# Kernel optimization log

Hardware: AMD Instinct MI355X
Metric: run time of the kernel (lower is better)

## Reference

```python
import jax, jax.numpy as jnp
from jax import lax
import numpy as np

N_TOTAL = 262144
NUM_SAMPLE = 1024
KNN_K = 16
NUM_CLASSES = 13
HIDDEN = 128
EPS = 1e-8


def _sqdist(a, b):
    # (Na,3),(Nb,3) -> (Na,Nb) squared euclidean; same argmin as torch.cdist
    return (jnp.sum(a * a, axis=1)[:, None]
            + jnp.sum(b * b, axis=1)[None, :]
            - 2.0 * a @ b.T)


def _farthest_point_sample(xyz, n_samples):
    # sequential FPS starting from index 0 (deterministic start)
    n = xyz.shape[0]

    def step(carry, _):
        min_d2, last = carry
        d2 = jnp.sum((xyz - xyz[last]) ** 2, axis=-1)
        min_d2 = jnp.minimum(min_d2, d2)
        nxt = jnp.argmax(min_d2).astype(jnp.int32)
        return (min_d2, nxt), nxt

    init = (jnp.full((n,), 1e10, dtype=xyz.dtype), jnp.int32(0))
    _, idxs = lax.scan(step, init, None, length=n_samples - 1)
    return jnp.concatenate([jnp.zeros((1,), jnp.int32), idxs])


def _compute_normals(pts, k):
    # PCA normal per point from its k nearest neighbors (self excluded)
    d2 = _sqdist(pts, pts)                      # (S,S), S=1024 -> small
    _, nbr_idx = lax.top_k(-d2, k + 1)
    nbr = pts[nbr_idx[:, 1:]]                   # (S,k,3)
    centered = nbr - jnp.mean(nbr, axis=1, keepdims=True)
    cov = jnp.einsum('ski,skj->sij', centered, centered) / (k - 1)
    _, eigvecs = jnp.linalg.eigh(cov)           # ascending eigenvalues
    normal = eigvecs[..., 0]                    # smallest-eigval eigenvector
    return normal / (jnp.linalg.norm(normal, axis=-1, keepdims=True) + EPS)


def _forward(gaussian_positions, gaussian_colors, W1, b1, W2, b2, W3, b3):
    sample_idx = _farthest_point_sample(gaussian_positions, NUM_SAMPLE)
    dxyz = gaussian_positions[sample_idx]       # (S,3)
    drgb = gaussian_colors[sample_idx]          # (S,3)
    dnrm = _compute_normals(dxyz, KNN_K)        # (S,3)
    feats = jnp.concatenate([dxyz, drgb, dnrm], axis=1)  # (S,9)

    # pointwise segmentation network (stand-in for PointNet++ get_model)
    h = jax.nn.relu(feats @ W1 + b1)
    h = jax.nn.relu(h @ W2 + b2)
    pred = h @ W3 + b3                          # (S, num_classes)

    feat_down = jax.nn.softmax(pred, axis=1)
    lbl_down = jnp.argmax(pred, axis=1)

    # 1-NN label propagation: streaming-min candidate (memory-bound)
    d2_full = _sqdist(gaussian_positions, dxyz)  # (N, S) ~ 1 GB
    nearest = jnp.argmin(d2_full, axis=1)
    return feat_down[nearest], lbl_down[nearest]


def setup_inputs() -> dict:
    key = jax.random.key(0)
    ks = jax.random.split(key, 8)
    pos = jax.random.normal(ks[0], (N_TOTAL, 3), jnp.float32)
    col = jax.random.uniform(ks[1], (N_TOTAL, 3), jnp.float32)
    W1 = jax.random.normal(ks[2], (9, HIDDEN), jnp.float32) / np.sqrt(9.0)
    b1 = jnp.zeros((HIDDEN,), jnp.float32)
    W2 = jax.random.normal(ks[3], (HIDDEN, HIDDEN), jnp.float32) / np.sqrt(HIDDEN)
    b2 = jnp.zeros((HIDDEN,), jnp.float32)
    W3 = jax.random.normal(ks[4], (HIDDEN, NUM_CLASSES), jnp.float32) / np.sqrt(HIDDEN)
    b3 = jnp.zeros((NUM_CLASSES,), jnp.float32)
    return {"gaussian_positions": pos, "gaussian_colors": col,
            "W1": W1, "b1": b1, "W2": W2, "b2": b2, "W3": W3, "b3": b3}


def reference(gaussian_positions, gaussian_colors, W1, b1, W2, b2, W3, b3):
    return _forward(gaussian_positions, gaussian_colors, W1, b1, W2, b2, W3, b3)
```

## Files before the change

### kernel.cpp

```cpp
#include <hip/hip_runtime.h>
#include <math.h>

#define N_TOTAL    262144
#define NUM_SAMPLE 1024
#define FPS_BLOCKS 64
#define FPS_THREADS 256
#define FPS_PPT (N_TOTAL / (FPS_BLOCKS * FPS_THREADS))
#define M_WAVE 4
#define POOL (FPS_BLOCKS * 4 * M_WAVE)
#define ENT_PER_T (POOL / FPS_THREADS)
#define QD (POOL / 64)
#define SEL_CAP 1023

__device__ __forceinline__ float addrn(float a, float b) { return __fadd_rn(a, b); }
__device__ __forceinline__ float subrn(float a, float b) { return __fsub_rn(a, b); }
__device__ __forceinline__ float mulrn(float a, float b) { return __fmul_rn(a, b); }

__device__ __forceinline__ float d2rn(float ax, float ay, float az,
                                      float bx, float by, float bz) {
  float dx = subrn(ax, bx), dy = subrn(ay, by), dz = subrn(az, bz);
  return addrn(addrn(mulrn(dx, dx), mulrn(dy, dy)), mulrn(dz, dz));
}

__device__ __forceinline__ bool lex_gt(float m1, unsigned i1, float m2, unsigned i2) {
  return (m1 > m2) || (m1 == m2 && i1 > i2);
}
__device__ __forceinline__ bool lex_ge(float m1, unsigned i1, float m2, unsigned i2) {
  return (m1 > m2) || (m1 == m2 && i1 >= i2);
}

template <int CTRL>
__device__ __forceinline__ int dpp_i(int x) {
  return __builtin_amdgcn_update_dpp(x, x, CTRL, 0xF, 0xF, false);
}
__device__ __forceinline__ float wave_fmax_bcast(float v) {
  v = fmaxf(v, __int_as_float(dpp_i<0x111>(__float_as_int(v))));
  v = fmaxf(v, __int_as_float(dpp_i<0x112>(__float_as_int(v))));
  v = fmaxf(v, __int_as_float(dpp_i<0x114>(__float_as_int(v))));
  v = fmaxf(v, __int_as_float(dpp_i<0x118>(__float_as_int(v))));
  v = fmaxf(v, __int_as_float(dpp_i<0x142>(__float_as_int(v))));
  v = fmaxf(v, __int_as_float(dpp_i<0x143>(__float_as_int(v))));
  return __int_as_float(__builtin_amdgcn_readlane(__float_as_int(v), 63));
}
__device__ __forceinline__ unsigned wave_umax_bcast(unsigned v) {
  unsigned o;
  o = (unsigned)dpp_i<0x111>((int)v); v = (o > v) ? o : v;
  o = (unsigned)dpp_i<0x112>((int)v); v = (o > v) ? o : v;
  o = (unsigned)dpp_i<0x114>((int)v); v = (o > v) ? o : v;
  o = (unsigned)dpp_i<0x118>((int)v); v = (o > v) ? o : v;
  o = (unsigned)dpp_i<0x142>((int)v); v = (o > v) ? o : v;
  o = (unsigned)dpp_i<0x143>((int)v); v = (o > v) ? o : v;
  return (unsigned)__builtin_amdgcn_readlane((int)v, 63);
}

__device__ __forceinline__ float slapy2f(float x, float y) {
  float xa = fabsf(x), ya = fabsf(y);
  float w = fmaxf(xa, ya), z = fminf(xa, ya);
  if (z == 0.f) return w;
  float t = z / w;
  return w * __fsqrt_rn(1.f + t * t);
}

__device__ __forceinline__ void slartgf(float f, float g, float& c, float& s, float& r) {
  if (g == 0.f) { c = 1.f; s = 0.f; r = f; }
  else if (f == 0.f) { c = 0.f; s = (g > 0.f) ? 1.f : -1.f; r = fabsf(g); }
  else {
    float d = __fsqrt_rn(f * f + g * g);
    c = fabsf(f) / d;
    r = (f >= 0.f) ? d : -d;
    s = g / r;
  }
}

__device__ void slaev2f(float a, float b, float c0, float& rt1, float& rt2,
                        float& cs1, float& sn1) {
  float sm = a + c0, df = a - c0;
  float adf = fabsf(df), tb = b + b, ab = fabsf(tb);
  float acmx, acmn;
  if (fabsf(a) > fabsf(c0)) { acmx = a; acmn = c0; } else { acmx = c0; acmn = a; }
  float rt;
  if (adf > ab)      { float t = ab / adf; rt = adf * __fsqrt_rn(1.f + t * t); }
  else if (adf < ab) { float t = adf / ab; rt = ab * __fsqrt_rn(1.f + t * t); }
  else               { rt = ab * __fsqrt_rn(2.f); }
  int sgn1;
  if (sm < 0.f)      { rt1 = 0.5f * (sm - rt); sgn1 = -1; rt2 = (acmx / rt1) * acmn - (b / rt1) * b; }
  else if (sm > 0.f) { rt1 = 0.5f * (sm + rt); sgn1 = 1;  rt2 = (acmx / rt1) * acmn - (b / rt1) * b; }
  else               { rt1 = 0.5f * rt; rt2 = -0.5f * rt; sgn1 = 1; }
  float cs; int sgn2;
  if (df >= 0.f) { cs = df + rt; sgn2 = 1; } else { cs = df - rt; sgn2 = -1; }
  float acs = fabsf(cs);
  if (acs > ab) {
    float ct = -tb / cs;
    sn1 = 1.f / __fsqrt_rn(1.f + ct * ct);
    cs1 = ct * sn1;
  } else {
    if (ab == 0.f) { cs1 = 1.f; sn1 = 0.f; }
    else { float tn = -cs / tb; cs1 = 1.f / __fsqrt_rn(1.f + tn * tn); sn1 = tn * cs1; }
  }
  if (sgn1 == sgn2) { float tn = cs1; cs1 = -sn1; sn1 = tn; }
}

#define D_(i) d[(i)-1]
#define E_(i) e[(i)-1]

__device__ void ssteqr3(float d[3], float e[2], float Z[3][3]) {
  const float eps    = 5.9604645e-08f;
  const float eps2   = 3.5527137e-15f;
  const float safmin = 1.17549435e-38f;
  const float ssfmax = 3.0744573e+18f;
  const float ssfmin = 3.0517578e-05f;
  const int n = 3;
  int jtot = 0, nmaxit = 90;
  int l1 = 1;

  while (true) {
    if (l1 > n) break;
    if (l1 > 1) E_(l1 - 1) = 0.f;
    int m = n;
    for (int mm = l1; mm <= n - 1; ++mm) {
      float tst = fabsf(E_(mm));
      if (tst == 0.f) { m = mm; break; }
      if (tst <= (__fsqrt_rn(fabsf(D_(mm))) * __fsqrt_rn(fabsf(D_(mm + 1)))) * eps) {
        E_(mm) = 0.f; m = mm; break;
      }
    }
    int l = l1, lsv = l, lend = m, lendsv = m;
    l1 = m + 1;
    if (lend == l) continue;

    float anorm = fabsf(D_(lend));
    for (int i2 = l; i2 <= lend - 1; ++i2) {
      anorm = fmaxf(anorm, fabsf(D_(i2)));
      anorm = fmaxf(anorm, fabsf(E_(i2)));
    }
    int iscale = 0;
    if (anorm == 0.f) continue;
    if (anorm > ssfmax) {
      iscale = 1; float mul = ssfmax / anorm;
      for (int i2 = l; i2 <= lend; ++i2) D_(i2) *= mul;
      for (int i2 = l; i2 <= lend - 1; ++i2) E_(i2) *= mul;
    } else if (anorm < ssfmin) {
      iscale = 2; float mul = ssfmin / anorm;
      for (int i2 = l; i2 <= lend; ++i2) D_(i2) *= mul;
      for (int i2 = l; i2 <= lend - 1; ++i2) E_(i2) *= mul;
    }

    if (fabsf(D_(lend)) < fabsf(D_(l))) { int t = l; l = lend; lend = t; }

    if (lend > l) {
      while (true) {
        int m2 = lend;
        if (l != lend) {
          for (int mm = l; mm <= lend - 1; ++mm) {
            float tst = fabsf(E_(mm)); tst = tst * tst;
            if (tst <= (eps2 * fabsf(D_(mm))) * fabsf(D_(mm + 1)) + safmin) { m2 = mm; break; }
          }
        }
        if (m2 < lend) E_(m2) = 0.f;
        float p = D_(l);
        if (m2 == l) { D_(l) = p; l = l + 1; if (l <= lend) continue; break; }
        if (m2 == l + 1) {
          float rt1, rt2, cc, ss;
          slaev2f(D_(l), E_(l), D_(l + 1), rt1, rt2, cc, ss);
          for (int i2 = 0; i2 < 3; ++i2) {
            float tmp = Z[i2][l];
            Z[i2][l]     = cc * tmp - ss * Z[i2][l - 1];
            Z[i2][l - 1] = ss * tmp + cc * Z[i2][l - 1];
          }
          D_(l) = rt1; D_(l + 1) = rt2; E_(l) = 0.f;
          l = l + 2; if (l <= lend) continue; break;
        }
        if (jtot == nmaxit) break;
        ++jtot;
        float g = (D_(l + 1) - p) / (2.f * E_(l));
        float r = slapy2f(g, 1.f);
        float sgn_rg = (g >= 0.f) ? r : -r;
        g = D_(m2) - p + E_(l) / (g + sgn_rg);
        float s = 1.f, c = 1.f;
        p = 0.f;
        float csv[2], ssv[2];
        for (int i2 = m2 - 1; i2 >= l; --i2) {
          float f = s * E_(i2);
          float b = c * E_(i2);
          slartgf(g, f, c, s, r);
          if (i2 != m2 - 1) E_(i2 + 1) = r;
          g = D_(i2 + 1) - p;
          r = (D_(i2) - g) * s + 2.f * c * b;
          p = s * r;
          D_(i2 + 1) = g + p;
          g = c * r - b;
          csv[i2 - l] = c; ssv[i2 - l] = -s;
        }
        for (int j = m2 - 1; j >= l; --j) {
          float ct = csv[j - l], st = ssv[j - l];
          for (int i2 = 0; i2 < 3; ++i2) {
            float tmp = Z[i2][j];
            Z[i2][j]     = ct * tmp - st * Z[i2][j - 1];
            Z[i2][j - 1] = st * tmp + ct * Z[i2][j - 1];
          }
        }
        D_(l) = D_(l) - p;
        E_(l) = g;
      }
    } else {
      while (true) {
        int m2 = lend;
        if (l != lend) {
          for (int mm = l; mm >= lend + 1; --mm) {
            float tst = fabsf(E_(mm - 1)); tst = tst * tst;
            if (tst <= (eps2 * fabsf(D_(mm))) * fabsf(D_(mm - 1)) + safmin) { m2 = mm; break; }
          }
        }
        if (m2 > lend) E_(m2 - 1) = 0.f;
        float p = D_(l);
        if (m2 == l) { D_(l) = p; l = l - 1; if (l >= lend) continue; break; }
        if (m2 == l - 1) {
          float rt1, rt2, cc, ss;
          slaev2f(D_(l - 1), E_(l - 1), D_(l), rt1, rt2, cc, ss);
          for (int i2 = 0; i2 < 3; ++i2) {
            float tmp = Z[i2][l - 1];
            Z[i2][l - 1] = cc * tmp - ss * Z[i2][l - 2];
            Z[i2][l - 2] = ss * tmp + cc * Z[i2][l - 2];
          }
          D_(l - 1) = rt1; D_(l) = rt2; E_(l - 1) = 0.f;
          l = l - 2; if (l >= lend) continue; break;
        }
        if (jtot == nmaxit) break;
        ++jtot;
        float g = (D_(l - 1) - p) / (2.f * E_(l - 1));
        float r = slapy2f(g, 1.f);
        float sgn_rg = (g >= 0.f) ? r : -r;
        g = D_(m2) - p + E_(l - 1) / (g + sgn_rg);
        float s = 1.f, c = 1.f;
        p = 0.f;
        float csv[2], ssv[2];
        for (int i2 = m2; i2 <= l - 1; ++i2) {
          float f = s * E_(i2);
          float b = c * E_(i2);
          slartgf(g, f, c, s, r);
          if (i2 != m2) E_(i2 - 1) = r;
          g = D_(i2) - p;
          r = (D_(i2 + 1) - g) * s + 2.f * c * b;
          p = s * r;
          D_(i2) = g + p;
          g = c * r - b;
          csv[i2 - m2] = c; ssv[i2 - m2] = s;
        }
        for (int j = m2; j <= l - 1; ++j) {
          float ct = csv[j - m2], st = ssv[j - m2];
          for (int i2 = 0; i2 < 3; ++i2) {
            float tmp = Z[i2][j];
            Z[i2][j]     = ct * tmp - st * Z[i2][j - 1];
            Z[i2][j - 1] = st * tmp + ct * Z[i2][j - 1];
          }
        }
        D_(l) = D_(l) - p;
        E_(l - 1) = g;
      }
    }
    if (iscale == 1) {
      float mul = anorm / ssfmax;
      for (int i2 = lsv; i2 <= lendsv; ++i2) D_(i2) *= mul;
      for (int i2 = lsv; i2 <= lendsv - 1; ++i2) E_(i2) *= mul;
    } else if (iscale == 2) {
      float mul = anorm / ssfmin;
      for (int i2 = lsv; i2 <= lendsv; ++i2) D_(i2) *= mul;
      for (int i2 = lsv; i2 <= lendsv - 1; ++i2) E_(i2) *= mul;
    }
  }
  for (int ii = 2; ii <= n; ++ii) {
    int i2 = ii - 1, k = i2;
    float p = D_(i2);
    for (int j = ii; j <= n; ++j) if (D_(j) < p) { k = j; p = D_(j); }
    if (k != i2) {
      D_(k) = D_(i2); D_(i2) = p;
      for (int rr = 0; rr < 3; ++rr) {
        float t = Z[rr][i2 - 1]; Z[rr][i2 - 1] = Z[rr][k - 1]; Z[rr][k - 1] = t;
      }
    }
  }
}

__device__ void eigh3_smallest(float a00, float a10, float a20, float a11, float a21, float a22,
                               float& nx, float& ny, float& nz) {
  float d[3], e[2];
  float Z[3][3] = {{1.f,0.f,0.f},{0.f,1.f,0.f},{0.f,0.f,1.f}};
  float tau, v2;
  {
    float alpha = a10, x = a20;
    float xnorm = fabsf(x);
    if (xnorm == 0.f) {
      tau = 0.f; v2 = 0.f;
      d[0] = a00; d[1] = a11; d[2] = a22;
      e[0] = alpha; e[1] = a21;
    } else {
      float beta = -copysignf(slapy2f(alpha, x), alpha);
      tau = (beta - alpha) / beta;
      v2 = x / (alpha - beta);
      float w0 = (tau * a11) + tau * (a21 * v2);
      float w1 = (tau * a21) + (tau * v2) * a22;
      float ac = (-0.5f * tau) * (w0 + w1 * v2);
      w0 = w0 + ac;
      w1 = w1 + ac * v2;
      d[0] = a00;
      d[1] = (a11 - w0) - w0;
      d[2] = (a22 - v2 * w1) - w1 * v2;
      e[0] = beta;
      e[1] = (a21 - v2 * w0) - w1;
    }
  }
  ssteqr3(d, e, Z);
  if (tau != 0.f) {
    for (int c = 0; c < 3; ++c) {
      float w = Z[1][c] + Z[2][c] * v2;
      float temp = (-tau) * w;
      Z[1][c] = Z[1][c] + temp;
      Z[2][c] = Z[2][c] + v2 * temp;
    }
  }
  nx = Z[0][0]; ny = Z[1][0]; nz = Z[2][0];
}

__global__ void k0_init(unsigned long long* cand, int* sample_idx) {
  int t = blockIdx.x * blockDim.x + threadIdx.x;
  if (t < 2 * POOL) cand[t] = 0ull;
  if (t == 0) sample_idx[0] = 0;
}

__global__ __launch_bounds__(FPS_THREADS, 1) void k1_fps(
    const float* __restrict__ pos,
    unsigned long long* __restrict__ cand,
    int* __restrict__ sample_idx) {
  __shared__ float4 sel4[SEL_CAP];
  __shared__ float act_x[POOL], act_y[POOL], act_z[POOL], act_md[POOL];
  __shared__ unsigned act_idf[POOL];
  __shared__ float thrT_md[FPS_THREADS];
  __shared__ unsigned thrT_idf[FPS_THREADS];
  __shared__ int sh_pc;

  const int tidx = threadIdx.x;
  const int lane = tidx & 63;
  const int gtid = blockIdx.x * FPS_THREADS + tidx;

  float px[FPS_PPT], py[FPS_PPT], pz[FPS_PPT], md[FPS_PPT];
#pragma unroll
  for (int k = 0; k < FPS_PPT; ++k) {
    int p = gtid + k * (FPS_BLOCKS * FPS_THREADS);
    px[k] = pos[3 * p]; py[k] = pos[3 * p + 1]; pz[k] = pos[3 * p + 2];
    md[k] = 1e10f;
  }
  const unsigned idf0 = 0x3FFFFFu - (unsigned)gtid;
  if (tidx == 0) sel4[0] = make_float4(pos[0], pos[1], pos[2], 0.f);
  __syncthreads();
  int sel_cnt = 1, total = 0, bt = 0;
  while (total < NUM_SAMPLE - 1) {
    ++bt;
    {
      float4 sc = sel4[0];
      for (int s = 0; s < sel_cnt; ++s) {
        float4 sn = (s + 1 < sel_cnt) ? sel4[s + 1] : sc;
#pragma unroll
        for (int k = 0; k < FPS_PPT; ++k)
          md[k] = fminf(md[k], d2rn(px[k], py[k], pz[k], sc.x, sc.y, sc.z));
        sc = sn;
      }
    }
    const unsigned tag = (unsigned)bt & 1023u;
    unsigned long long* setbase = cand + (size_t)(bt & 1) * POOL;
    {
      float wmd[FPS_PPT];
#pragma unroll
      for (int k = 0; k < FPS_PPT; ++k) wmd[k] = md[k];
      unsigned long long mypub = 0ull;
      for (int r = 0; r < M_WAVE; ++r) {
        float bm = wmd[0]; unsigned bidf = idf0;
#pragma unroll
        for (int k = 1; k < FPS_PPT; ++k) {
          unsigned idfk = idf0 - ((unsigned)k << 14);
          if (wmd[k] > bm || (wmd[k] == bm && idfk > bidf)) { bm = wmd[k]; bidf = idfk; }
        }
        float wmx = wave_fmax_bcast(bm);
        unsigned tb = (bm == wmx) ? bidf : 0u;
        unsigned widf = wave_umax_bcast(tb);
        if (lane == r)
          mypub = ((unsigned long long)__float_as_uint(wmx) << 32) |
                  ((unsigned long long)widf << 10);
#pragma unroll
        for (int k = 0; k < FPS_PPT; ++k) {
          unsigned idfk = idf0 - ((unsigned)k << 14);
          if (wmd[k] == wmx && idfk == widf) wmd[k] = -1.f;
        }
      }
      if (lane < M_WAVE)
        __hip_atomic_store(setbase + blockIdx.x * (4 * M_WAVE) + (tidx >> 6) * M_WAVE + lane,
                           mypub | tag, __ATOMIC_RELAXED, __HIP_MEMORY_SCOPE_AGENT);
    }
    const int base_w = tidx * ENT_PER_T;
    {
      float cmd[ENT_PER_T]; unsigned cidf[ENT_PER_T];
      float cx[ENT_PER_T], cy[ENT_PER_T], cz[ENT_PER_T];
      unsigned done = 0;
      while (done != 0xFu) {
#pragma unroll
        for (int j = 0; j < ENT_PER_T; ++j) {
          if (!((done >> j) & 1u)) {
            unsigned long long v = __hip_atomic_load(setbase + base_w + j,
                                                     __ATOMIC_RELAXED, __HIP_MEMORY_SCOPE_AGENT);
            if ((unsigned)(v & 1023ull) == tag) {
              done |= 1u << j;
              cmd[j] = __uint_as_float((unsigned)(v >> 32));
              cidf[j] = (unsigned)((v >> 10) & 0x3FFFFFull);
              int gidx = 0x3FFFFF - (int)cidf[j];
              cx[j] = pos[3 * gidx]; cy[j] = pos[3 * gidx + 1]; cz[j] = pos[3 * gidx + 2];
            }
          }
        }
        if (done != 0xFu) __builtin_amdgcn_s_sleep(1);
      }
#pragma unroll
      for (int j = 0; j < ENT_PER_T; ++j) {
        int e = j * FPS_THREADS + tidx;
        act_x[e] = cx[j]; act_y[e] = cy[j]; act_z[e] = cz[j];
        act_md[e] = cmd[j]; act_idf[e] = cidf[j];
      }
      thrT_md[tidx] = cmd[ENT_PER_T - 1]; thrT_idf[tidx] = cidf[ENT_PER_T - 1];
    }
    __syncthreads();
    const int room = (NUM_SAMPLE - 1) - total;
    if (tidx < 64) {
      float q_md[QD], q_x[QD], q_y[QD], q_z[QD];
      unsigned q_idf[QD];
#pragma unroll
      for (int r = 0; r < QD; ++r) {
        int e2 = lane + 64 * r;
        q_x[r] = act_x[e2]; q_y[r] = act_y[e2]; q_z[r] = act_z[e2];
        q_md[r] = act_md[e2]; q_idf[r] = act_idf[e2];
      }
      float rm = thrT_md[lane]; unsigned ri = thrT_idf[lane];
#pragma unroll
      for (int r = 1; r < 4; ++r) {
        float m = thrT_md[lane + 64 * r]; unsigned ii = thrT_idf[lane + 64 * r];
        if (lex_gt(m, ii, rm, ri)) { rm = m; ri = ii; }
      }
      float Tmd = wave_fmax_bcast(rm);
      unsigned tbT = (rm == Tmd) ? ri : 0u;
      unsigned Tidf = wave_umax_bcast(tbT);

      int picks = 0;
      float X = 1e30f, Y = 1e30f, Z = 1e30f;
      for (;;) {
        float bm = -1.f; unsigned bidf = 0u;
        float bx = 0.f, by = 0.f, bz = 0.f;
#pragma unroll
        for (int j = 0; j < QD; ++j) {
          float nd = fminf(q_md[j], d2rn(q_x[j], q_y[j], q_z[j], X, Y, Z));
          q_md[j] = nd;
          if (lex_gt(nd, q_idf[j], bm, bidf)) {
            bm = nd; bidf = q_idf[j]; bx = q_x[j]; by = q_y[j]; bz = q_z[j];
          }
        }
        float wmx = wave_fmax_bcast(bm);
        unsigned long long ball = __ballot(bm == wmx);
        unsigned widf; int owner;
        if (__builtin_popcountll(ball) == 1) {
          owner = __builtin_ctzll(ball);
          widf = (unsigned)__builtin_amdgcn_readlane((int)bidf, owner);
        } else {
          unsigned tb = (bm == wmx) ? bidf : 0u;
          widf = wave_umax_bcast(tb);
          owner = __builtin_ctzll(__ballot(bm == wmx && bidf == widf));
        }
        if (picks >= room) break;
        if (!lex_ge(wmx, widf, Tmd, Tidf)) break;
        X = __int_as_float(__builtin_amdgcn_readlane(__float_as_int(bx), owner));
        Y = __int_as_float(__builtin_amdgcn_readlane(__float_as_int(by), owner));
        Z = __int_as_float(__builtin_amdgcn_readlane(__float_as_int(bz), owner));
        if (lane == 0) {
          sel4[picks] = make_float4(X, Y, Z, 0.f);
          if (blockIdx.x == 0) sample_idx[1 + total + picks] = 0x3FFFFF - (int)widf;
        }
        ++picks;
      }
      if (lane == 0) sh_pc = picks;
    }
    __syncthreads();
    sel_cnt = sh_pc;
    total += sel_cnt;
  }
}

__global__ __launch_bounds__(256) void k2a_knn(
    const float* __restrict__ pos, const float* __restrict__ col,
    const int* __restrict__ sample_idx,
    float4* __restrict__ sp4g, float* __restrict__ feats9) {
  __shared__ float4 sp[NUM_SAMPLE];
  const int tid = threadIdx.x, lane = tid & 63, wv = tid >> 6;
  for (int i = tid; i < NUM_SAMPLE; i += 256) {
    int idx = sample_idx[i];
    float x = pos[3 * idx], y = pos[3 * idx + 1], z = pos[3 * idx + 2];
    float nrm = addrn(addrn(mulrn(x, x), mulrn(y, y)), mulrn(z, z));
    float4 v = make_float4(x, y, z, nrm);
    sp[i] = v;
    if (blockIdx.x == 0) sp4g[i] = v;
  }
  __syncthreads();
  for (int it = 0; it < 4; ++it) {
    const int r = blockIdx.x * 16 + wv * 4 + it;
    float4 pr = sp[r];
    unsigned long long kk[16];
#pragma unroll
    for (int k = 0; k < 16; ++k) {
      int j = lane + 64 * k;
      float4 q = sp[j];
      float dot = fmaf(pr.z, q.z, fmaf(pr.y, q.y, mulrn(pr.x, q.x)));
      float d2 = subrn(addrn(pr.w, q.w), mulrn(2.f, dot));
      unsigned b = __float_as_uint(d2);
      unsigned sbits = (b & 0x80000000u) ? ~b : (b | 0x80000000u);
      kk[k] = ((unsigned long long)sbits << 32) | (unsigned)j;
    }
    int bi[17];
#pragma unroll
    for (int rsel = 0; rsel < 17; ++rsel) {
      unsigned long long best = 0xFFFFFFFFFFFFFFFFull;
#pragma unroll
      for (int k = 0; k < 16; ++k) best = (kk[k] < best) ? kk[k] : best;
#pragma unroll
      for (int mk = 1; mk < 64; mk <<= 1) {
        unsigned long long o = (unsigned long long)__shfl_xor((long long)best, mk, 64);
        best = (o < best) ? o : best;
      }
      int j = (int)(best & 0xFFFFFFFFull);
      bi[rsel] = j;
#pragma unroll
      for (int k = 0; k < 16; ++k)
        if (((j >> 6) == k) && ((j & 63) == lane)) kk[k] = 0xFFFFFFFFFFFFFFFFull;
    }
    float mx = 0.f, my = 0.f, mz = 0.f;
#pragma unroll
    for (int k = 1; k <= 16; ++k) {
      float4 q = sp[bi[k]];
      mx = addrn(mx, q.x); my = addrn(my, q.y); mz = addrn(mz, q.z);
    }
    mx = mulrn(mx, 0.0625f); my = mulrn(my, 0.0625f); mz = mulrn(mz, 0.0625f);
    float c00 = 0.f, c01 = 0.f, c02 = 0.f, c11 = 0.f, c12 = 0.f, c22 = 0.f;
#pragma unroll
    for (int k = 1; k <= 16; ++k) {
      float4 q = sp[bi[k]];
      float dx = subrn(q.x, mx), dy = subrn(q.y, my), dz = subrn(q.z, mz);
      c00 = addrn(c00, mulrn(dx, dx)); c01 = addrn(c01, mulrn(dx, dy));
      c02 = addrn(c02, mulrn(dx, dz)); c11 = addrn(c11, mulrn(dy, dy));
      c12 = addrn(c12, mulrn(dy, dz)); c22 = addrn(c22, mulrn(dz, dz));
    }
    c00 /= 15.f; c01 /= 15.f; c02 /= 15.f; c11 /= 15.f; c12 /= 15.f; c22 /= 15.f;

    float n0, n1, n2;
    eigh3_smallest(c00, c01, c02, c11, c12, c22, n0, n1, n2);
    float nn = __fsqrt_rn(addrn(addrn(mulrn(n0, n0), mulrn(n1, n1)), mulrn(n2, n2)));
    float den = addrn(nn, 1e-8f);
    n0 /= den; n1 /= den; n2 /= den;

    if (lane == 0) {
      int myidx = sample_idx[r];
      float* f = feats9 + r * 9;
      f[0] = pr.x; f[1] = pr.y; f[2] = pr.z;
      f[3] = col[3 * myidx]; f[4] = col[3 * myidx + 1]; f[5] = col[3 * myidx + 2];
      f[6] = n0; f[7] = n1; f[8] = n2;
    }
  }
}

__global__ __launch_bounds__(64) void k2b_mlp(
    const float* __restrict__ W1, const float* __restrict__ b1,
    const float* __restrict__ W2, const float* __restrict__ b2,
    const float* __restrict__ W3, const float* __restrict__ b3,
    const float* __restrict__ feats9,
    float* __restrict__ featd, int* __restrict__ lbl) {
  __shared__ float hbuf[64][129];
  const int tid = threadIdx.x;
  const int r = blockIdx.x * 64 + tid;
  float f9[9];
#pragma unroll
  for (int k = 0; k < 9; ++k) f9[k] = feats9[r * 9 + k];
  for (int jo = 0; jo < 128; ++jo) {
    float acc = 0.f;
#pragma unroll
    for (int k = 0; k < 9; ++k) acc = fmaf(f9[k], W1[k * 128 + jo], acc);
    acc += b1[jo];
    hbuf[tid][jo] = fmaxf(acc, 0.f);
  }
  float pd[13];
#pragma unroll
  for (int c = 0; c < 13; ++c) pd[c] = 0.f;
  for (int io = 0; io < 128; io += 16) {
    float acc[16];
#pragma unroll
    for (int t = 0; t < 16; ++t) acc[t] = 0.f;
    for (int j = 0; j < 128; ++j) {
      float hj = hbuf[tid][j];
#pragma unroll
      for (int t = 0; t < 16; ++t) acc[t] = fmaf(hj, W2[j * 128 + io + t], acc[t]);
    }
#pragma unroll
    for (int t = 0; t < 16; ++t) {
      float h2 = fmaxf(acc[t] + b2[io + t], 0.f);
#pragma unroll
      for (int c = 0; c < 13; ++c) pd[c] = fmaf(h2, W3[(io + t) * 13 + c], pd[c]);
    }
  }
#pragma unroll
  for (int c = 0; c < 13; ++c) pd[c] += b3[c];
  float mmax = pd[0];
#pragma unroll
  for (int c = 1; c < 13; ++c) mmax = fmaxf(mmax, pd[c]);
  float es = 0.f, ev[13];
#pragma unroll
  for (int c = 0; c < 13; ++c) { ev[c] = expf(pd[c] - mmax); es += ev[c]; }
#pragma unroll
  for (int c = 0; c < 13; ++c) featd[r * 13 + c] = ev[c] / es;
  int am = 0; float bv = pd[0];
#pragma unroll
  for (int c = 1; c < 13; ++c) { if (pd[c] > bv) { bv = pd[c]; am = c; } }
  lbl[r] = am;
}

__global__ __launch_bounds__(256) void k3_assign(
    const float* __restrict__ pos,
    const float4* __restrict__ sp4g,
    const float* __restrict__ featd,
    const int* __restrict__ lbl,
    float* __restrict__ out) {
  __shared__ float4 sp[NUM_SAMPLE];
  for (int i = threadIdx.x; i < NUM_SAMPLE; i += 256) sp[i] = sp4g[i];
  __syncthreads();
  int i = blockIdx.x * 256 + threadIdx.x;
  float x = pos[3 * i], y = pos[3 * i + 1], z = pos[3 * i + 2];
  float an = addrn(addrn(mulrn(x, x), mulrn(y, y)), mulrn(z, z));
  float bestd = 3.402823466e+38f; int bestj = 0;
#pragma unroll 4
  for (int j = 0; j < NUM_SAMPLE; ++j) {
    float4 q = sp[j];
    float dot = fmaf(z, q.z, fmaf(y, q.y, mulrn(x, q.x)));
    float d2 = subrn(addrn(an, q.w), mulrn(2.f, dot));
    if (d2 < bestd) { bestd = d2; bestj = j; }
  }
  const float* fr = featd + bestj * 13;
  float* o = out + (size_t)i * 13;
#pragma unroll
  for (int c = 0; c < 13; ++c) o[c] = fr[c];
  out[(size_t)N_TOTAL * 13 + i] = (float)lbl[bestj];
}

extern "C" void kernel_launch(void* const* d_in, const int* in_sizes, int n_in,
                              void* d_out, int out_size, void* d_ws, size_t ws_size,
                              hipStream_t stream) {
  (void)in_sizes; (void)n_in; (void)out_size; (void)ws_size;
  const float* pos = (const float*)d_in[0];
  const float* col = (const float*)d_in[1];
  const float* W1 = (const float*)d_in[2];
  const float* b1 = (const float*)d_in[3];
  const float* W2 = (const float*)d_in[4];
  const float* b2 = (const float*)d_in[5];
  const float* W3 = (const float*)d_in[6];
  const float* b3 = (const float*)d_in[7];
  float* out = (float*)d_out;

  char* w = (char*)d_ws;
  unsigned long long* cand = (unsigned long long*)(w);
  int* sample_idx = (int*)(w + 65536);
  float4* sp4g = (float4*)(w + 73728);
  float* featd = (float*)(w + 90112);
  int* lbl = (int*)(w + 143360);
  float* feats9 = (float*)(w + 147456);

  k0_init<<<16, 256, 0, stream>>>(cand, sample_idx);
  k1_fps<<<FPS_BLOCKS, FPS_THREADS, 0, stream>>>(pos, cand, sample_idx);
  k2a_knn<<<64, 256, 0, stream>>>(pos, col, sample_idx, sp4g, feats9);
  k2b_mlp<<<16, 64, 0, stream>>>(W1, b1, W2, b2, W3, b3, feats9, featd, lbl);
  k3_assign<<<N_TOTAL / 256, 256, 0, stream>>>(pos, sp4g, featd, lbl, out);
}
```

Measured before the change: 1.710 ms.

## Double per-wave FPS candidates and pack candidate pool into float4 LDS

```diff
diff --git a/kernel.cpp b/kernel.cpp
--- a/kernel.cpp
+++ b/kernel.cpp
@@ -6,10 +6,10 @@
 #define FPS_BLOCKS 64
 #define FPS_THREADS 256
 #define FPS_PPT (N_TOTAL / (FPS_BLOCKS * FPS_THREADS))
-#define M_WAVE 4
+#define M_WAVE 8
 #define POOL (FPS_BLOCKS * 4 * M_WAVE)
 #define ENT_PER_T (POOL / FPS_THREADS)
-#define QD (POOL / 64)
+#define QL (POOL / 64)
 #define SEL_CAP 1023
 
 __device__ __forceinline__ float addrn(float a, float b) { return __fadd_rn(a, b); }
@@ -332,7 +332,7 @@
     unsigned long long* __restrict__ cand,
     int* __restrict__ sample_idx) {
   __shared__ float4 sel4[SEL_CAP];
-  __shared__ float act_x[POOL], act_y[POOL], act_z[POOL], act_md[POOL];
+  __shared__ float4 act4[POOL];
   __shared__ unsigned act_idf[POOL];
   __shared__ float thrT_md[FPS_THREADS];
   __shared__ unsigned thrT_idf[FPS_THREADS];
@@ -395,16 +395,15 @@
         __hip_atomic_store(setbase + blockIdx.x * (4 * M_WAVE) + (tidx >> 6) * M_WAVE + lane,
                            mypub | tag, __ATOMIC_RELAXED, __HIP_MEMORY_SCOPE_AGENT);
     }
-    const int base_w = tidx * ENT_PER_T;
     {
       float cmd[ENT_PER_T]; unsigned cidf[ENT_PER_T];
       float cx[ENT_PER_T], cy[ENT_PER_T], cz[ENT_PER_T];
       unsigned done = 0;
-      while (done != 0xFu) {
+      while (done != 0xFFu) {
 #pragma unroll
         for (int j = 0; j < ENT_PER_T; ++j) {
           if (!((done >> j) & 1u)) {
-            unsigned long long v = __hip_atomic_load(setbase + base_w + j,
+            unsigned long long v = __hip_atomic_load(setbase + j * FPS_THREADS + tidx,
                                                      __ATOMIC_RELAXED, __HIP_MEMORY_SCOPE_AGENT);
             if ((unsigned)(v & 1023ull) == tag) {
               done |= 1u << j;
@@ -415,26 +414,30 @@
             }
           }
         }
-        if (done != 0xFu) __builtin_amdgcn_s_sleep(1);
+        if (done != 0xFFu) __builtin_amdgcn_s_sleep(1);
       }
 #pragma unroll
       for (int j = 0; j < ENT_PER_T; ++j) {
         int e = j * FPS_THREADS + tidx;
-        act_x[e] = cx[j]; act_y[e] = cy[j]; act_z[e] = cz[j];
-        act_md[e] = cmd[j]; act_idf[e] = cidf[j];
-      }
-      thrT_md[tidx] = cmd[ENT_PER_T - 1]; thrT_idf[tidx] = cidf[ENT_PER_T - 1];
+        act4[e] = make_float4(cx[j], cy[j], cz[j], cmd[j]);
+        act_idf[e] = cidf[j];
+      }
+      float tm = -1.f; unsigned ti = 0u;
+      if ((tidx & 7) == 7) {
+#pragma unroll
+        for (int j = 0; j < ENT_PER_T; ++j)
+          if (lex_gt(cmd[j], cidf[j], tm, ti)) { tm = cmd[j]; ti = cidf[j]; }
+      }
+      thrT_md[tidx] = tm; thrT_idf[tidx] = ti;
     }
     __syncthreads();
     const int room = (NUM_SAMPLE - 1) - total;
     if (tidx < 64) {
-      float q_md[QD], q_x[QD], q_y[QD], q_z[QD];
-      unsigned q_idf[QD];
-#pragma unroll
-      for (int r = 0; r < QD; ++r) {
+      float q_md[QL]; unsigned q_idf[QL];
+#pragma unroll
+      for (int r = 0; r < QL; ++r) {
         int e2 = lane + 64 * r;
-        q_x[r] = act_x[e2]; q_y[r] = act_y[e2]; q_z[r] = act_z[e2];
-        q_md[r] = act_md[e2]; q_idf[r] = act_idf[e2];
+        q_md[r] = act4[e2].w; q_idf[r] = act_idf[e2];
       }
       float rm = thrT_md[lane]; unsigned ri = thrT_idf[lane];
 #pragma unroll
@@ -452,11 +455,12 @@
         float bm = -1.f; unsigned bidf = 0u;
         float bx = 0.f, by = 0.f, bz = 0.f;
 #pragma unroll
-        for (int j = 0; j < QD; ++j) {
-          float nd = fminf(q_md[j], d2rn(q_x[j], q_y[j], q_z[j], X, Y, Z));
+        for (int j = 0; j < QL; ++j) {
+          float4 a = act4[lane + 64 * j];
+          float nd = fminf(q_md[j], d2rn(a.x, a.y, a.z, X, Y, Z));
           q_md[j] = nd;
           if (lex_gt(nd, q_idf[j], bm, bidf)) {
-            bm = nd; bidf = q_idf[j]; bx = q_x[j]; by = q_y[j]; bz = q_z[j];
+            bm = nd; bidf = q_idf[j]; bx = a.x; by = a.y; bz = a.z;
           }
         }
         float wmx = wave_fmax_bcast(bm);
```

Measured after the change: 2.390 ms. 39.8% more time.

## Publish more FPS candidates per wave and compact pool by threshold

Applied to the files above, without the earlier changes.

```diff
diff --git a/kernel.cpp b/kernel.cpp
--- a/kernel.cpp
+++ b/kernel.cpp
@@ -6,10 +6,11 @@
 #define FPS_BLOCKS 64
 #define FPS_THREADS 256
 #define FPS_PPT (N_TOTAL / (FPS_BLOCKS * FPS_THREADS))
-#define M_WAVE 4
+#define M_WAVE 8
 #define POOL (FPS_BLOCKS * 4 * M_WAVE)
 #define ENT_PER_T (POOL / FPS_THREADS)
-#define QD (POOL / 64)
+#define CAP 1024
+#define QD 16
 #define SEL_CAP 1023
 
 __device__ __forceinline__ float addrn(float a, float b) { return __fadd_rn(a, b); }
@@ -332,14 +333,15 @@
     unsigned long long* __restrict__ cand,
     int* __restrict__ sample_idx) {
   __shared__ float4 sel4[SEL_CAP];
-  __shared__ float act_x[POOL], act_y[POOL], act_z[POOL], act_md[POOL];
-  __shared__ unsigned act_idf[POOL];
-  __shared__ float thrT_md[FPS_THREADS];
-  __shared__ unsigned thrT_idf[FPS_THREADS];
-  __shared__ int sh_pc;
+  __shared__ float act_x[CAP], act_y[CAP], act_z[CAP], act_md[CAP];
+  __shared__ unsigned act_idf[CAP];
+  __shared__ float wred_m7[4], wred_m4[4];
+  __shared__ unsigned wred_i7[4], wred_i4[4];
+  __shared__ int sh_cnt, sh_pc;
 
   const int tidx = threadIdx.x;
   const int lane = tidx & 63;
+  const int wv = tidx >> 6;
   const int gtid = blockIdx.x * FPS_THREADS + tidx;
 
   float px[FPS_PPT], py[FPS_PPT], pz[FPS_PPT], md[FPS_PPT];
@@ -392,15 +394,15 @@
         }
       }
       if (lane < M_WAVE)
-        __hip_atomic_store(setbase + blockIdx.x * (4 * M_WAVE) + (tidx >> 6) * M_WAVE + lane,
+        __hip_atomic_store(setbase + blockIdx.x * (4 * M_WAVE) + wv * M_WAVE + lane,
                            mypub | tag, __ATOMIC_RELAXED, __HIP_MEMORY_SCOPE_AGENT);
     }
     const int base_w = tidx * ENT_PER_T;
+    float cmd[ENT_PER_T]; unsigned cidf[ENT_PER_T];
+    float cx[ENT_PER_T], cy[ENT_PER_T], cz[ENT_PER_T];
     {
-      float cmd[ENT_PER_T]; unsigned cidf[ENT_PER_T];
-      float cx[ENT_PER_T], cy[ENT_PER_T], cz[ENT_PER_T];
       unsigned done = 0;
-      while (done != 0xFu) {
+      while (done != 0xFFu) {
 #pragma unroll
         for (int j = 0; j < ENT_PER_T; ++j) {
           if (!((done >> j) & 1u)) {
@@ -415,37 +417,75 @@
             }
           }
         }
-        if (done != 0xFu) __builtin_amdgcn_s_sleep(1);
-      }
+        if (done != 0xFFu) __builtin_amdgcn_s_sleep(1);
+      }
+    }
+    {
+      float m7 = cmd[ENT_PER_T - 1]; unsigned i7 = cidf[ENT_PER_T - 1];
+      float w7 = wave_fmax_bcast(m7);
+      unsigned t7 = (m7 == w7) ? i7 : 0u;
+      unsigned wi7 = wave_umax_bcast(t7);
+      float m4 = cmd[4]; unsigned i4 = cidf[4];
+      float w4 = wave_fmax_bcast(m4);
+      unsigned t4 = (m4 == w4) ? i4 : 0u;
+      unsigned wi4 = wave_umax_bcast(t4);
+      if (lane == 0) { wred_m7[wv] = w7; wred_i7[wv] = wi7; wred_m4[wv] = w4; wred_i4[wv] = wi4; }
+      if (tidx == 0) sh_cnt = 0;
+    }
+    __syncthreads();
+    float Tmd = wred_m7[0]; unsigned Tidf = wred_i7[0];
+    float T2m = wred_m4[0]; unsigned T2i = wred_i4[0];
+#pragma unroll
+    for (int w = 1; w < 4; ++w) {
+      if (lex_gt(wred_m7[w], wred_i7[w], Tmd, Tidf)) { Tmd = wred_m7[w]; Tidf = wred_i7[w]; }
+      if (lex_gt(wred_m4[w], wred_i4[w], T2m, T2i)) { T2m = wred_m4[w]; T2i = wred_i4[w]; }
+    }
+    unsigned fl = 0; int myc = 0;
+#pragma unroll
+    for (int j = 0; j < ENT_PER_T; ++j) {
+      if (lex_ge(cmd[j], cidf[j], Tmd, Tidf)) { fl |= 1u << j; ++myc; }
+    }
+    int base = atomicAdd(&sh_cnt, myc);
+    __syncthreads();
+    const int cnt = sh_cnt;
+    const bool ovf = (cnt > CAP);
+    if (!ovf) {
+      int s = base;
 #pragma unroll
       for (int j = 0; j < ENT_PER_T; ++j) {
-        int e = j * FPS_THREADS + tidx;
-        act_x[e] = cx[j]; act_y[e] = cy[j]; act_z[e] = cz[j];
-        act_md[e] = cmd[j]; act_idf[e] = cidf[j];
-      }
-      thrT_md[tidx] = cmd[ENT_PER_T - 1]; thrT_idf[tidx] = cidf[ENT_PER_T - 1];
+        if ((fl >> j) & 1u) {
+          act_x[s] = cx[j]; act_y[s] = cy[j]; act_z[s] = cz[j];
+          act_md[s] = cmd[j]; act_idf[s] = cidf[j];
+          ++s;
+        }
+      }
+    } else {
+#pragma unroll
+      for (int k = 0; k < 4; ++k) {
+        int s = tidx * 4 + k;
+        act_x[s] = cx[k]; act_y[s] = cy[k]; act_z[s] = cz[k];
+        act_md[s] = cmd[k]; act_idf[s] = cidf[k];
+      }
     }
     __syncthreads();
     const int room = (NUM_SAMPLE - 1) - total;
     if (tidx < 64) {
+      const int cnt_eff = ovf ? CAP : cnt;
+      const float Bm = ovf ? T2m : Tmd;
+      const unsigned Bi = ovf ? T2i : Tidf;
       float q_md[QD], q_x[QD], q_y[QD], q_z[QD];
       unsigned q_idf[QD];
 #pragma unroll
       for (int r = 0; r < QD; ++r) {
         int e2 = lane + 64 * r;
-        q_x[r] = act_x[e2]; q_y[r] = act_y[e2]; q_z[r] = act_z[e2];
-        q_md[r] = act_md[e2]; q_idf[r] = act_idf[e2];
-      }
-      float rm = thrT_md[lane]; unsigned ri = thrT_idf[lane];
-#pragma unroll
-      for (int r = 1; r < 4; ++r) {
-        float m = thrT_md[lane + 64 * r]; unsigned ii = thrT_idf[lane + 64 * r];
-        if (lex_gt(m, ii, rm, ri)) { rm = m; ri = ii; }
-      }
-      float Tmd = wave_fmax_bcast(rm);
-      unsigned tbT = (rm == Tmd) ? ri : 0u;
-      unsigned Tidf = wave_umax_bcast(tbT);
-
+        if (e2 < cnt_eff) {
+          q_x[r] = act_x[e2]; q_y[r] = act_y[e2]; q_z[r] = act_z[e2];
+          q_md[r] = act_md[e2]; q_idf[r] = act_idf[e2];
+        } else {
+          q_x[r] = 0.f; q_y[r] = 0.f; q_z[r] = 0.f;
+          q_md[r] = -1.f; q_idf[r] = 0u;
+        }
+      }
       int picks = 0;
       float X = 1e30f, Y = 1e30f, Z = 1e30f;
       for (;;) {
@@ -471,7 +511,7 @@
           owner = __builtin_ctzll(__ballot(bm == wmx && bidf == widf));
         }
         if (picks >= room) break;
-        if (!lex_ge(wmx, widf, Tmd, Tidf)) break;
+        if (!lex_ge(wmx, widf, Bm, Bi)) break;
         X = __int_as_float(__builtin_amdgcn_readlane(__float_as_int(bx), owner));
         Y = __int_as_float(__builtin_amdgcn_readlane(__float_as_int(by), owner));
         Z = __int_as_float(__builtin_amdgcn_readlane(__float_as_int(bz), owner));
```

New measurement: 1.782 ms. +4.2%, slower.
